# Kernel tuning notes

Measured on AMD Instinct MI355X. Metric: run time of the kernel, lower is better.

## Reference

```python
import jax, jax.numpy as jnp
import numpy as np

NX, NY = 512, 512
FNUM, GNUM = 120, 120
NA = 1.35
WAVELENGTH = NX * NA / 100.0  # chosen so normalized period = 100
N_LIQUID = 1.44
M_RED = 0.25
LOW_LIGHT_THRES = 1e-3
SRC_STEEP = 8.0
RESIST_STEEP = 30.0
RESIST_INT = 0.225
DOSES = (0.98, 1.0, 1.02)
SRC_GRID = 13

X1 = NX // 2 - FNUM; X2 = NX // 2 + FNUM + 1
Y1 = NY // 2 - GNUM; Y2 = NY // 2 + GNUM + 1
_PER_X = NX / (WAVELENGTH / NA)
_PER_Y = NY / (WAVELENGTH / NA)
NORM_SPEC = _PER_X * _PER_Y
DFMDG = 1.0 / NORM_SPEC
_fm = (np.arange(X1, X2) - NX // 2) / _PER_X
_gm = (np.arange(Y1, Y2) - NY // 2) / _PER_Y
_FM, _GM = np.meshgrid(_fm, _gm)  # 'xy' indexing, shape [2*GNUM+1, 2*FNUM+1]
FM = jnp.asarray(_FM, jnp.float32)
GM = jnp.asarray(_GM, jnp.float32)


def cal_pupil(fg2):
    # obliquity factor; pupil phase is identically zero in this module
    num = 1.0 - (M_RED ** 2) * (NA ** 2) * fg2
    den = 1.0 - (NA / N_LIQUID) ** 2 * fg2
    return jnp.sqrt(jnp.sqrt(num / den))


def setup_inputs() -> dict:
    key = jax.random.key(0)
    g = np.linspace(-1.0, 1.0, SRC_GRID, dtype=np.float32)
    fxg, fyg = np.meshgrid(g, g)
    r = np.sqrt(fxg ** 2 + fyg ** 2)
    data = ((r >= 0.6) & (r <= 0.9)).astype(np.float32)  # annular source
    # sigmoid activation init: +1 where lit, -1 elsewhere (zeros, set 2 where data>0.5, sub 1)
    params = 2.0 * data - 1.0
    mask_value = jax.random.uniform(key, (NY, NX), jnp.float32)
    return {
        "mask_value": mask_value,
        "source_params": jnp.asarray(params, jnp.float32),
        "source_fx": jnp.asarray(fxg.reshape(-1), jnp.float32),
        "source_fy": jnp.asarray(fyg.reshape(-1), jnp.float32),
    }


def _forward(mask_value, source_params, source_fx, source_fy):
    # source activation + low-light pruning (masked_select expressed as zero-weighting)
    val = jax.nn.sigmoid(SRC_STEEP * source_params).reshape(-1)  # [S]
    valid = val >= LOW_LIGHT_THRES
    w = jnp.where(valid, val, 0.0)
    weight = jnp.sum(w)

    # normalization intensity (detached in the original)
    fxy2 = source_fx ** 2 + source_fy ** 2
    obl = cal_pupil(jnp.where(valid, fxy2, 0.0))
    norm_I = jax.lax.stop_gradient(
        N_LIQUID * DFMDG ** 2 * jnp.sum(w * (NORM_SPEC * obl) ** 2) / weight
    )

    # shifted pupil per source point over the mask frequency window
    F = FM[None, :, :] + source_fx[:, None, None]  # [S, Gy, Gx]
    G = GM[None, :, :] + source_fy[:, None, None]
    rho2 = F * F + G * G                            # == mask_fg2m + 2(fx*fm+fy*gm) + fxy2
    vmask = rho2 <= 1.0
    pupil = jnp.where(vmask, cal_pupil(jnp.where(vmask, rho2, 0.0)), 0.0)  # [S, Gy, Gx]

    S = w.shape[0]
    Is, Rs = [], []
    for d in DOSES:
        fv = jnp.fft.fftshift(jnp.fft.fft2(jnp.fft.ifftshift(mask_value * d)))
        win = fv[Y1:Y2, X1:X2]                      # [Gy, Gx] complex
        tempH = win[None, :, :] * pupil.astype(jnp.complex64)  # masked spectrum*pupil
        e = jnp.zeros((S, NY, NX), jnp.complex64).at[:, Y1:Y2, X1:X2].set(tempH)
        AA = jnp.fft.fftshift(jnp.fft.ifft2(e), axes=(-2, -1))
        I2 = AA.real ** 2 + AA.imag ** 2            # |AA * conj(AA)|
        intensity = jnp.einsum('s,syx->yx', w, I2) / weight / norm_I
        Is.append(intensity)
        Rs.append(jax.nn.sigmoid(RESIST_STEEP * (intensity - RESIST_INT)))
    # [2, 3, NY, NX]: [0] = aerial intensity per dose, [1] = resist image per dose
    return jnp.stack([jnp.stack(Is), jnp.stack(Rs)])


def reference(mask_value, source_params, source_fx, source_fy):
    return _forward(mask_value, source_params, source_fx, source_fy)
```

## Files before the change

### kernel.cpp

```cpp
#include <hip/hip_runtime.h>
#include <hip/hip_fp16.h>


#define SPLIT 8

static const size_t O_BAR  = 4096;
static const size_t O_ACC  = 32768;
static const size_t ACC_BYTES = (size_t)SPLIT * 512 * 512 * 4;
static const size_t O_WIN  = O_ACC + ACC_BYTES;
static const size_t O_R1   = O_WIN + 464896;
static const size_t O_T2   = O_R1 + 987136;
static const size_t SLOT_BYTES = (size_t)512 * 244 * 4;

__device__ inline void st_sys_f(float* p, float v) {
  __hip_atomic_store((unsigned*)p, __float_as_uint(v),
                     __ATOMIC_RELAXED, __HIP_MEMORY_SCOPE_SYSTEM);
}
__device__ inline float ld_sys_f(const float* p) {
  return __uint_as_float(__hip_atomic_load((const unsigned*)p,
                     __ATOMIC_RELAXED, __HIP_MEMORY_SCOPE_SYSTEM));
}
__device__ inline void st_sys_i(int* p, int v) {
  __hip_atomic_store(p, v, __ATOMIC_RELAXED, __HIP_MEMORY_SCOPE_SYSTEM);
}
__device__ inline int ld_sys_i(const int* p) {
  return __hip_atomic_load(p, __ATOMIC_RELAXED, __HIP_MEMORY_SCOPE_SYSTEM);
}
__device__ inline void st_sys_f2(float2* p, float2 v) {
  union { float2 f; unsigned long long u; } c; c.f = v;
  __hip_atomic_store((unsigned long long*)p, c.u,
                     __ATOMIC_RELAXED, __HIP_MEMORY_SCOPE_SYSTEM);
}
__device__ inline float2 ld_sys_f2(const float2* p) {
  union { unsigned long long u; float2 f; } c;
  c.u = __hip_atomic_load((const unsigned long long*)p,
                     __ATOMIC_RELAXED, __HIP_MEMORY_SCOPE_SYSTEM);
  return c.f;
}
__device__ inline void st_sys_f4(void* p, float4 v) {
  union { float2 f; unsigned long long u; } a, b;
  a.f = make_float2(v.x, v.y); b.f = make_float2(v.z, v.w);
  unsigned long long* q = (unsigned long long*)p;
  __hip_atomic_store(q,     a.u, __ATOMIC_RELAXED, __HIP_MEMORY_SCOPE_SYSTEM);
  __hip_atomic_store(q + 1, b.u, __ATOMIC_RELAXED, __HIP_MEMORY_SCOPE_SYSTEM);
}
__device__ inline __half2 ld_sys_h2(const __half2* p) {
  union { unsigned u; __half2 h; } c;
  c.u = __hip_atomic_load((const unsigned*)p,
                     __ATOMIC_RELAXED, __HIP_MEMORY_SCOPE_SYSTEM);
  return c.h;
}

__device__ inline float2 cadd(float2 a, float2 b){ return make_float2(a.x+b.x, a.y+b.y); }
__device__ inline float2 csub(float2 a, float2 b){ return make_float2(a.x-b.x, a.y-b.y); }
__device__ inline float2 cmul(float2 a, float2 b){
  return make_float2(fmaf(a.x, b.x, -(a.y*b.y)), fmaf(a.x, b.y, a.y*b.x));
}
__device__ inline float2 twsgn(float2 t, int S) {
  return make_float2(t.x, (S > 0) ? t.y : -t.y);
}

__device__ inline void gbar(char* bar, unsigned nblk, unsigned& ep) {
  __syncthreads();
  ep++;
  if (threadIdx.x == 0) {
    const unsigned target = ep;
    const unsigned g    = blockIdx.x >> 5;
    const unsigned ngrp = nblk >> 5;
    unsigned* gcnt = (unsigned*)(bar + (size_t)g * 256);
    unsigned* ggen = (unsigned*)(bar + 8192 + (size_t)g * 256);
    unsigned* rcnt = (unsigned*)(bar + 16384);
    unsigned* rgen = (unsigned*)(bar + 16640);
    asm volatile("s_waitcnt vmcnt(0)" ::: "memory");
    unsigned old = __hip_atomic_fetch_add(gcnt, 1u, __ATOMIC_RELAXED,
                                          __HIP_MEMORY_SCOPE_SYSTEM);
    if (old == 31u) {
      __hip_atomic_store(gcnt, 0u, __ATOMIC_RELAXED, __HIP_MEMORY_SCOPE_SYSTEM);
      unsigned r = __hip_atomic_fetch_add(rcnt, 1u, __ATOMIC_RELAXED,
                                          __HIP_MEMORY_SCOPE_SYSTEM);
      if (r == ngrp - 1u) {
        __hip_atomic_store(rcnt, 0u, __ATOMIC_RELAXED, __HIP_MEMORY_SCOPE_SYSTEM);
        __hip_atomic_store(rgen, target, __ATOMIC_RELAXED,
                           __HIP_MEMORY_SCOPE_SYSTEM);
      } else {
        while (__hip_atomic_load(rgen, __ATOMIC_RELAXED,
                                 __HIP_MEMORY_SCOPE_SYSTEM) < target)
          __builtin_amdgcn_s_sleep(1);
      }
      __hip_atomic_store(ggen, target, __ATOMIC_RELAXED,
                         __HIP_MEMORY_SCOPE_SYSTEM);
    } else {
      while (__hip_atomic_load(ggen, __ATOMIC_RELAXED,
                               __HIP_MEMORY_SCOPE_SYSTEM) < target)
        __builtin_amdgcn_s_sleep(2);
    }
  }
  __syncthreads();
}

__device__ inline void build_twt(float2* twt) {
  for (int k = (int)threadIdx.x; k < 512; k += 256) {
    double a = 6.283185307179586476925286766559 * (double)k / 512.0;
    twt[k] = make_float2((float)cos(a), (float)sin(a));
  }
}

template<int S, bool ZTOP>
__device__ inline void dft8(float2 v[8]) {
  const float sg = (float)S;
  const float C7 = 0.7071067811865476f;
  float2 t0, t1, t2, t3, t4, t5, t6, t7;
  if (ZTOP) {
    t0 = v[0]; t4 = v[0];
    t1 = v[1]; t5 = v[1];
    t2 = v[2]; t6 = v[2];
    t3 = v[3]; t7 = v[3];
  } else {
    t0=cadd(v[0],v[4]); t4=csub(v[0],v[4]);
    t1=cadd(v[1],v[5]); t5=csub(v[1],v[5]);
    t2=cadd(v[2],v[6]); t6=csub(v[2],v[6]);
    t3=cadd(v[3],v[7]); t7=csub(v[3],v[7]);
  }
  t5 = make_float2(C7*(t5.x - sg*t5.y), C7*(t5.y + sg*t5.x));
  t6 = make_float2(-sg*t6.y, sg*t6.x);
  t7 = make_float2(C7*(-t7.x - sg*t7.y), C7*(sg*t7.x - t7.y));
  float2 u0=cadd(t0,t2), u2=csub(t0,t2);
  float2 u1=cadd(t1,t3), u3=csub(t1,t3);
  u3 = make_float2(-sg*u3.y, sg*u3.x);
  float2 u4=cadd(t4,t6), u6=csub(t4,t6);
  float2 u5=cadd(t5,t7), u7=csub(t5,t7);
  u7 = make_float2(-sg*u7.y, sg*u7.x);
  v[0]=cadd(u0,u1); v[4]=csub(u0,u1);
  v[2]=cadd(u2,u3); v[6]=csub(u2,u3);
  v[1]=cadd(u4,u5); v[5]=csub(u4,u5);
  v[3]=cadd(u6,u7); v[7]=csub(u6,u7);
}

template<int S, bool ZTOP>
__device__ inline void wfft512(float2 v[8], int lane, float2* xch,
                               const float2* twt) {
  const int p2 = lane & 7, u0 = lane >> 3;
  dft8<S, ZTOP>(v);
  { float2 t1 = twsgn(twt[lane], S), acc = t1;
    v[1] = cmul(v[1], acc);
    #pragma unroll
    for (int u = 2; u < 8; u++) { acc = cmul(acc, t1); v[u] = cmul(v[u], acc); } }
  __builtin_amdgcn_wave_barrier();
  #pragma unroll
  for (int u = 0; u < 8; u++) xch[u*68 + p2*8 + u0] = v[u];
  __builtin_amdgcn_wave_barrier();
  { const float4* rp = (const float4*)(xch + u0*68 + p2*8);
    #pragma unroll
    for (int q = 0; q < 4; q++) {
      float4 t = rp[q];
      v[2*q]   = make_float2(t.x, t.y);
      v[2*q+1] = make_float2(t.z, t.w);
    } }
  dft8<S, false>(v);
  { float2 t1 = twsgn(twt[p2 << 3], S), acc = t1;
    v[1] = cmul(v[1], acc);
    #pragma unroll
    for (int u = 2; u < 8; u++) { acc = cmul(acc, t1); v[u] = cmul(v[u], acc); } }
  __builtin_amdgcn_wave_barrier();
  #pragma unroll
  for (int u = 0; u < 8; u++) xch[u*68 + lane] = v[u];
  __builtin_amdgcn_wave_barrier();
  { const float4* rp = (const float4*)(xch + p2*68 + u0*8);
    #pragma unroll
    for (int q = 0; q < 4; q++) {
      float4 t = rp[q];
      v[2*q]   = make_float2(t.x, t.y);
      v[2*q+1] = make_float2(t.z, t.w);
    } }
  dft8<S, false>(v);
}

__global__ void __launch_bounds__(256, 4)
k_fused(const float* __restrict__ mask, const float* __restrict__ prm,
        const float* __restrict__ sfx, const float* __restrict__ sfy,
        char* ws, float2* R1t, float2* Wg, __half2* T2, float* acc,
        float* out, int CH) {
  const int t = threadIdx.x, lane = t & 63, wv = t >> 6;
  const unsigned nblk = gridDim.x;
  char* bar = ws + O_BAR;
  unsigned ep = 0;
  __shared__ __align__(16) float2 lds[4*544];
  __shared__ __align__(16) float2 twt[512];
  __shared__ float FMt[241];
  build_twt(twt);
  if (t < 241) FMt[t] = (float)(((double)(t - 120)) / 100.0);
  float2* const xch = lds + wv*544;

  if (blockIdx.x == 0) {
    float*  sw  = (float*)lds;
    float*  sxx = sw + 192; float* syy = sxx + 192; float* scw = syy + 192;
    double* so  = (double*)(sw + 768);
    int*    skp = (int*)(so + 176);
    if (t < 169) {
      float p = prm[t];
      float val = 1.f / (1.f + __expf(-8.f * p));
      float w = (val >= 0.001f) ? val : 0.f;
      double o = 0.0; float fx = 0.f, fy = 0.f;
      if (w > 0.f) {
        fx = sfx[t]; fy = sfy[t];
        double f2 = (double)fx*(double)fx + (double)fy*(double)fy;
        o = (double)w * sqrt((1.0 - 0.11390625 * f2) / (1.0 - 0.87890625 * f2));
      }
      sw[t] = w; so[t] = o; sxx[t] = fx; syy[t] = fy;
    }
    __syncthreads();
    if (t < 169) {
      float w = sw[t];
      int keep = 0; float cw = w;
      if (w > 0.f) {
        float fx = sxx[t], fy = syy[t];
        int pr = -1;
        for (int s2 = 0; s2 < 169; s2++) {
          if (sw[s2] > 0.f && fabsf(sxx[s2] + fx) < 1e-5f
                           && fabsf(syy[s2] + fy) < 1e-5f) { pr = s2; break; }
        }
        if (pr < 0 || pr == t) keep = 1;
        else if (pr > t) { keep = 1; cw = w + sw[pr]; }
      }
      skp[t] = keep; scw[t] = cw;
    }
    __syncthreads();
    if (t == 0) {
      float* wsfw = (float*)ws;
      double Sden = 0.0; int c = 0;
      for (int s = 0; s < 169; s++) {
        Sden += so[s];
        if (skp[s]) {
          st_sys_f(wsfw + 64 + c,  scw[s]);
          st_sys_f(wsfw + 320 + c, sxx[s]);
          st_sys_f(wsfw + 576 + c, syy[s]);
          c++;
        }
      }
      st_sys_i((int*)ws, c);
      st_sys_f(wsfw + 1, (float)(1.0 / (262144.0 * 1.44 * Sden)));
    }
    __syncthreads();
  }
  {
    int rb0, step;
    if (nblk > 128) { rb0 = (int)blockIdx.x - 1; step = (int)nblk - 1; }
    else            { rb0 = (int)blockIdx.x;     step = (int)nblk; }
    if (rb0 >= 0) {
      for (int rb = rb0; rb < 128; rb += step) {
        int y = rb * 4 + wv;
        float2 v[8];
        #pragma unroll
        for (int q = 0; q < 8; q++) v[q] = make_float2(mask[y*512 + 64*q + lane], 0.f);
        wfft512<-1, false>(v, lane, xch, twt);
        #pragma unroll
        for (int u = 0; u < 8; u++) {
          int k = (lane>>3) + 8*(lane&7) + 64*u;
          int beta = (k >= 392) ? (k - 392) : ((k <= 120) ? (k + 120) : -1);
          if (beta >= 0) st_sys_f2(R1t + beta*512 + y, v[u]);
        }
      }
    }
  }
  gbar(bar, nblk, ep);

  for (int jb = blockIdx.x; jb < 61; jb += nblk) {
    int j = jb * 4 + wv;
    float2 v[8];
    #pragma unroll
    for (int q = 0; q < 8; q++)
      v[q] = (j < 241) ? ld_sys_f2(R1t + j*512 + 64*q + lane)
                       : make_float2(0.f, 0.f);
    wfft512<-1, false>(v, lane, xch, twt);
    if (j < 241) {
      #pragma unroll
      for (int u = 0; u < 8; u++) {
        int k = (lane>>3) + 8*(lane&7) + 64*u;
        int alpha = (k >= 392) ? (k - 392) : ((k <= 120) ? (k + 120) : -1);
        if (alpha >= 0) st_sys_f2(Wg + alpha*241 + j, v[u]);
      }
    }
  }
  gbar(bar, nblk, ep);

  const float* wsf = (const float*)ws;
  const int count = ld_sys_i((const int*)ws);
  int nb = (count + CH - 1) / CH;
  if (nb < 1) nb = 1;
  for (int bi = 0; bi < nb; bi++) {
    const int base = bi * CH;
    int active = count - base;
    if (active > CH) active = CH;
    if (active < 0) active = 0;
    const int ntask = active * 31;

    for (int task = blockIdx.x; task < ntask; task += nblk) {
      int sic  = task / 31;
      int tile = task % 31;
      int slot = base + sic;
      float fx = ld_sys_f(wsf + 320 + slot), fy = ld_sys_f(wsf + 576 + slot);
      float sqw = __fsqrt_rn(ld_sys_f(wsf + 64 + slot)) * 0.001953125f;
      #pragma unroll
      for (int ph = 0; ph < 2; ph++) {
        int alpha = tile*8 + ph*4 + wv;
        bool arow = (alpha < 241);
        float Gf = __fadd_rn(arow ? FMt[alpha] : 0.f, fy);
        float g2 = __fmul_rn(Gf, Gf);
        bool active_row = arow && (g2 <= 1.0f);
        float2 v[8];
        #pragma unroll
        for (int q = 0; q < 8; q++) v[q] = make_float2(0.f, 0.f);
        if (active_row) {
          #pragma unroll
          for (int q = 0; q < 4; q++) {
            int n = 64*q + lane;
            if (n < 241) {
              float Ff = __fadd_rn(FMt[n], fx);
              float r2 = __fadd_rn(__fmul_rn(Ff, Ff), g2);
              if (r2 <= 1.0f) {
                float num = fmaf(-0.11390625f, r2, 1.0f);
                float den = fmaf(-0.87890625f, r2, 1.0f);
                float P = __fsqrt_rn(__fsqrt_rn(__fdividef(num, den))) * sqw;
                float2 Wv = ld_sys_f2(Wg + alpha*241 + n);
                v[q] = make_float2(P * Wv.x, P * Wv.y);
              }
            }
          }
          wfft512<1, true>(v, lane, xch, twt);
        }
        #pragma unroll
        for (int u = 0; u < 8; u++) {
          int xx = (lane>>3) + 8*(lane&7) + 64*u;
          xch[xx] = v[u];
        }
        __syncthreads();
        int colb = tile*8 + ph*4;
        if (colb < 244) {
          #pragma unroll
          for (int r = 0; r < 2; r++) {
            int x = t + 256*r;
            union { __half2 h[4]; float4 f; } uu;
            #pragma unroll
            for (int wvi = 0; wvi < 4; wvi++) {
              float2 a = lds[wvi*544 + x];
              uu.h[wvi] = __floats2half2_rn(a.x, a.y);
            }
            st_sys_f4(T2 + ((size_t)sic*512 + x)*244 + colb, uu.f);
          }
        }
        __syncthreads();
      }
    }
    gbar(bar, nblk, ep);

    for (int unit = blockIdx.x; unit < 1024; unit += nblk) {
      int part = unit & 7;
      int x = (unit >> 3) * 4 + wv;
      float av[8] = {0.f,0.f,0.f,0.f,0.f,0.f,0.f,0.f};
      int sic = part;
      bool act = (sic < CH) && (base + sic < count);
      __half2 pv[4] = {{0.f,0.f},{0.f,0.f},{0.f,0.f},{0.f,0.f}};
      if (act) {
        const __half2* row = T2 + ((size_t)sic*512 + x)*244;
        #pragma unroll
        for (int q = 0; q < 4; q++) {
          int n = 64*q + lane;
          pv[q] = (n < 241) ? ld_sys_h2(row + n) : __half2{0.f, 0.f};
        }
      }
      while (act) {
        float2 v[8];
        #pragma unroll
        for (int q = 0; q < 4; q++) v[q] = __half22float2(pv[q]);
        #pragma unroll
        for (int q = 4; q < 8; q++) v[q] = make_float2(0.f, 0.f);
        int nsic = sic + SPLIT;
        act = (nsic < CH) && (base + nsic < count);
        if (act) {
          const __half2* row = T2 + ((size_t)nsic*512 + x)*244;
          #pragma unroll
          for (int q = 0; q < 4; q++) {
            int n = 64*q + lane;
            pv[q] = (n < 241) ? ld_sys_h2(row + n) : __half2{0.f, 0.f};
          }
        }
        wfft512<1, true>(v, lane, xch, twt);
        #pragma unroll
        for (int u = 0; u < 8; u++)
          av[u] += fmaf(v[u].x, v[u].x, v[u].y*v[u].y);
        sic = nsic;
      }
      float* a = acc + ((size_t)part << 18) + (size_t)x * 512;
      int y0 = (lane>>3) + 8*(lane&7);
      if (bi == 0) {
        #pragma unroll
        for (int u = 0; u < 8; u++) st_sys_f(a + y0 + 64*u, av[u]);
      } else {
        #pragma unroll
        for (int u = 0; u < 8; u++) {
          float prev = ld_sys_f(a + y0 + 64*u);
          st_sys_f(a + y0 + 64*u, prev + av[u]);
        }
      }
    }
    gbar(bar, nblk, ep);
  }

  {
    float scale = ld_sys_f(wsf + 1);
    float (*tile2)[33] = reinterpret_cast<float(*)[33]>((float*)lds);
    const float dd[3] = {0.9604f, 1.0f, 1.0404f};
    int tx = t & 31, ty0 = t >> 5;
    for (int tb = blockIdx.x; tb < 256; tb += nblk) {
      int x0 = (tb & 15) * 32, y0 = (tb >> 4) * 32;
      #pragma unroll
      for (int r = 0; r < 4; r++) {
        int i = ty0 + 8*r;
        const float* ap = acc + (size_t)(x0 + i)*512 + y0 + tx;
        float s = 0.f;
        #pragma unroll
        for (int p = 0; p < SPLIT; p++) s += ld_sys_f(ap + ((size_t)p << 18));
        tile2[i][tx] = s;
      }
      __syncthreads();
      #pragma unroll
      for (int r = 0; r < 4; r++) {
        int yy = ty0 + 8*r;
        float I = scale * tile2[tx][yy];
        int o = (y0 + yy)*512 + x0 + tx;
        #pragma unroll
        for (int d = 0; d < 3; d++) {
          float Ik = dd[d] * I;
          out[(size_t)d*262144 + o] = Ik;
          out[(size_t)(3+d)*262144 + o] = 1.f / (1.f + __expf(-30.f*(Ik - 0.225f)));
        }
      }
      __syncthreads();
    }
  }
}

extern "C" void kernel_launch(void* const* d_in, const int* in_sizes, int n_in,
                              void* d_out, int out_size, void* d_ws, size_t ws_size,
                              hipStream_t stream) {
  (void)in_sizes; (void)n_in; (void)out_size;
  const float* mask = (const float*)d_in[0];
  const float* prm  = (const float*)d_in[1];
  const float* sfx  = (const float*)d_in[2];
  const float* sfy  = (const float*)d_in[3];
  float* out = (float*)d_out;
  char*  ws  = (char*)d_ws;

  float*   acc = (float*)(ws + O_ACC);
  float2*  Wg  = (float2*)(ws + O_WIN);
  float2*  R1t = (float2*)(ws + O_R1);
  __half2* T2  = (__half2*)(ws + O_T2);

  size_t avail = (ws_size > O_T2) ? (ws_size - O_T2) : 0;
  int CH = (int)(avail / SLOT_BYTES);
  if (CH > 169) CH = 169;
  if (CH < 1)   CH = 1;

  static int grid_blocks = 0;
  if (grid_blocks == 0) {
    int nbk = 0;
    if (hipOccupancyMaxActiveBlocksPerMultiprocessor(
            &nbk, (const void*)k_fused, 256, 0) != hipSuccess || nbk < 1)
      nbk = 1;
    if (nbk > 1) nbk -= 1;
    int ncu = 256;
    hipDeviceProp_t prop;
    int dev = 0;
    if (hipGetDevice(&dev) == hipSuccess &&
        hipGetDeviceProperties(&prop, dev) == hipSuccess &&
        prop.multiProcessorCount > 0)
      ncu = prop.multiProcessorCount;
    long g = (long)nbk * (long)ncu;
    if (g > 1024) g = 1024;
    g &= ~31L;
    if (g < 32) g = 32;
    grid_blocks = (int)g;
  }

  hipMemsetAsync(ws + O_BAR, 0, 24576, stream);

  k_fused<<<dim3(grid_blocks), dim3(256), 0, stream>>>(
      mask, prm, sfx, sfy, ws, R1t, Wg, T2, acc, out, CH);
}
```

Measured before the change: 152.1 us.

## Coalesce global stores via LDS transposes and widen T2 row layout

Routes the R1t and Wg transpose writes through LDS so each thread stores contiguous runs instead of strided scattered 8-byte stores. The stage-3 task split is reorganised so each block processes one column group of 4 per wave over 64 tasks, and the T2 row pitch is padded to 256 so stage-4 loads become 16-byte contiguous per lane. Accumulator writes and the final reduction are also vectorised to float2 after an LDS reshuffle. This adds extra LDS traffic and barriers, and changes task granularity, which may affect load balance.

Result: slower. 159.7 us (+5.0%).

```diff
diff --git a/kernel.cpp b/kernel.cpp
--- a/kernel.cpp
+++ b/kernel.cpp
@@ -10,7 +10,7 @@
 static const size_t O_WIN  = O_ACC + ACC_BYTES;
 static const size_t O_R1   = O_WIN + 464896;
 static const size_t O_T2   = O_R1 + 987136;
-static const size_t SLOT_BYTES = (size_t)512 * 244 * 4;
+static const size_t SLOT_BYTES = (size_t)512 * 256 * 4;
 
 __device__ inline void st_sys_f(float* p, float v) {
   __hip_atomic_store((unsigned*)p, __float_as_uint(v),
@@ -36,6 +36,10 @@
   c.u = __hip_atomic_load((const unsigned long long*)p,
                      __ATOMIC_RELAXED, __HIP_MEMORY_SCOPE_SYSTEM);
   return c.f;
+}
+__device__ inline unsigned long long ld_sys_u64(const void* p) {
+  return __hip_atomic_load((const unsigned long long*)p,
+                     __ATOMIC_RELAXED, __HIP_MEMORY_SCOPE_SYSTEM);
 }
 __device__ inline void st_sys_f4(void* p, float4 v) {
   union { float2 f; unsigned long long u; } a, b;
@@ -43,12 +47,6 @@
   unsigned long long* q = (unsigned long long*)p;
   __hip_atomic_store(q,     a.u, __ATOMIC_RELAXED, __HIP_MEMORY_SCOPE_SYSTEM);
   __hip_atomic_store(q + 1, b.u, __ATOMIC_RELAXED, __HIP_MEMORY_SCOPE_SYSTEM);
-}
-__device__ inline __half2 ld_sys_h2(const __half2* p) {
-  union { unsigned u; __half2 h; } c;
-  c.u = __hip_atomic_load((const unsigned*)p,
-                     __ATOMIC_RELAXED, __HIP_MEMORY_SCOPE_SYSTEM);
-  return c.h;
 }
 
 __device__ inline float2 cadd(float2 a, float2 b){ return make_float2(a.x+b.x, a.y+b.y); }
@@ -191,6 +189,7 @@
   if (t < 241) FMt[t] = (float)(((double)(t - 120)) / 100.0);
   float2* const xch = lds + wv*544;
 
+  __syncthreads();
   if (blockIdx.x == 0) {
     float*  sw  = (float*)lds;
     float*  sxx = sw + 192; float* syy = sxx + 192; float* scw = syy + 192;
@@ -257,8 +256,15 @@
         for (int u = 0; u < 8; u++) {
           int k = (lane>>3) + 8*(lane&7) + 64*u;
           int beta = (k >= 392) ? (k - 392) : ((k <= 120) ? (k + 120) : -1);
-          if (beta >= 0) st_sys_f2(R1t + beta*512 + y, v[u]);
-        }
+          if (beta >= 0) xch[beta] = v[u];
+        }
+        __syncthreads();
+        if (t < 241) {
+          float2* dst = R1t + t*512 + rb*4;
+          #pragma unroll
+          for (int w = 0; w < 4; w++) st_sys_f2(dst + w, lds[w*544 + t]);
+        }
+        __syncthreads();
       }
     }
   }
@@ -272,14 +278,21 @@
       v[q] = (j < 241) ? ld_sys_f2(R1t + j*512 + 64*q + lane)
                        : make_float2(0.f, 0.f);
     wfft512<-1, false>(v, lane, xch, twt);
-    if (j < 241) {
-      #pragma unroll
-      for (int u = 0; u < 8; u++) {
-        int k = (lane>>3) + 8*(lane&7) + 64*u;
-        int alpha = (k >= 392) ? (k - 392) : ((k <= 120) ? (k + 120) : -1);
-        if (alpha >= 0) st_sys_f2(Wg + alpha*241 + j, v[u]);
-      }
-    }
+    #pragma unroll
+    for (int u = 0; u < 8; u++) {
+      int k = (lane>>3) + 8*(lane&7) + 64*u;
+      int alpha = (k >= 392) ? (k - 392) : ((k <= 120) ? (k + 120) : -1);
+      if (alpha >= 0) xch[alpha] = v[u];
+    }
+    __syncthreads();
+    {
+      int nj = 241 - jb*4; if (nj > 4) nj = 4;
+      if (t < 241) {
+        float2* dst = Wg + t*241 + jb*4;
+        for (int w = 0; w < nj; w++) st_sys_f2(dst + w, lds[w*544 + t]);
+      }
+    }
+    __syncthreads();
   }
   gbar(bar, nblk, ep);
 
@@ -292,97 +305,85 @@
     int active = count - base;
     if (active > CH) active = CH;
     if (active < 0) active = 0;
-    const int ntask = active * 31;
+    const int ntask = active * 64;
 
     for (int task = blockIdx.x; task < ntask; task += nblk) {
-      int sic  = task / 31;
-      int tile = task % 31;
+      int sic = task >> 6;
+      int g   = task & 63;
       int slot = base + sic;
       float fx = ld_sys_f(wsf + 320 + slot), fy = ld_sys_f(wsf + 576 + slot);
       float sqw = __fsqrt_rn(ld_sys_f(wsf + 64 + slot)) * 0.001953125f;
+      int alpha = 64*wv + g;
+      bool arow = (alpha < 241);
+      float Gf = __fadd_rn(arow ? FMt[alpha] : 0.f, fy);
+      float g2 = __fmul_rn(Gf, Gf);
+      bool active_row = arow && (g2 <= 1.0f);
+      float2 v[8];
       #pragma unroll
-      for (int ph = 0; ph < 2; ph++) {
-        int alpha = tile*8 + ph*4 + wv;
-        bool arow = (alpha < 241);
-        float Gf = __fadd_rn(arow ? FMt[alpha] : 0.f, fy);
-        float g2 = __fmul_rn(Gf, Gf);
-        bool active_row = arow && (g2 <= 1.0f);
-        float2 v[8];
-        #pragma unroll
-        for (int q = 0; q < 8; q++) v[q] = make_float2(0.f, 0.f);
-        if (active_row) {
-          #pragma unroll
-          for (int q = 0; q < 4; q++) {
-            int n = 64*q + lane;
-            if (n < 241) {
-              float Ff = __fadd_rn(FMt[n], fx);
-              float r2 = __fadd_rn(__fmul_rn(Ff, Ff), g2);
-              if (r2 <= 1.0f) {
-                float num = fmaf(-0.11390625f, r2, 1.0f);
-                float den = fmaf(-0.87890625f, r2, 1.0f);
-                float P = __fsqrt_rn(__fsqrt_rn(__fdividef(num, den))) * sqw;
-                float2 Wv = ld_sys_f2(Wg + alpha*241 + n);
-                v[q] = make_float2(P * Wv.x, P * Wv.y);
-              }
+      for (int q = 0; q < 8; q++) v[q] = make_float2(0.f, 0.f);
+      if (active_row) {
+        #pragma unroll
+        for (int q = 0; q < 4; q++) {
+          int n = 64*q + lane;
+          if (n < 241) {
+            float Ff = __fadd_rn(FMt[n], fx);
+            float r2 = __fadd_rn(__fmul_rn(Ff, Ff), g2);
+            if (r2 <= 1.0f) {
+              float num = fmaf(-0.11390625f, r2, 1.0f);
+              float den = fmaf(-0.87890625f, r2, 1.0f);
+              float P = __fsqrt_rn(__fsqrt_rn(__fdividef(num, den))) * sqw;
+              float2 Wv = ld_sys_f2(Wg + alpha*241 + n);
+              v[q] = make_float2(P * Wv.x, P * Wv.y);
             }
           }
-          wfft512<1, true>(v, lane, xch, twt);
-        }
-        #pragma unroll
-        for (int u = 0; u < 8; u++) {
-          int xx = (lane>>3) + 8*(lane&7) + 64*u;
-          xch[xx] = v[u];
-        }
-        __syncthreads();
-        int colb = tile*8 + ph*4;
-        if (colb < 244) {
-          #pragma unroll
-          for (int r = 0; r < 2; r++) {
-            int x = t + 256*r;
-            union { __half2 h[4]; float4 f; } uu;
-            #pragma unroll
-            for (int wvi = 0; wvi < 4; wvi++) {
-              float2 a = lds[wvi*544 + x];
-              uu.h[wvi] = __floats2half2_rn(a.x, a.y);
-            }
-            st_sys_f4(T2 + ((size_t)sic*512 + x)*244 + colb, uu.f);
-          }
-        }
-        __syncthreads();
-      }
+        }
+        wfft512<1, true>(v, lane, xch, twt);
+      }
+      #pragma unroll
+      for (int u = 0; u < 8; u++) {
+        int xx = (lane>>3) + 8*(lane&7) + 64*u;
+        xch[xx] = v[u];
+      }
+      __syncthreads();
+      #pragma unroll
+      for (int r = 0; r < 2; r++) {
+        int x = t + 256*r;
+        union { __half2 h[4]; float4 f; } uu;
+        #pragma unroll
+        for (int wvi = 0; wvi < 4; wvi++) {
+          float2 a = lds[wvi*544 + x];
+          uu.h[wvi] = __floats2half2_rn(a.x, a.y);
+        }
+        st_sys_f4(T2 + ((size_t)sic*512 + x)*256 + 4*g, uu.f);
+      }
+      __syncthreads();
     }
     gbar(bar, nblk, ep);
 
-    for (int unit = blockIdx.x; unit < 1024; unit += nblk) {
-      int part = unit & 7;
+    for (int unit = blockIdx.x; unit < 128*SPLIT; unit += nblk) {
+      int part = unit & (SPLIT-1);
       int x = (unit >> 3) * 4 + wv;
       float av[8] = {0.f,0.f,0.f,0.f,0.f,0.f,0.f,0.f};
       int sic = part;
       bool act = (sic < CH) && (base + sic < count);
-      __half2 pv[4] = {{0.f,0.f},{0.f,0.f},{0.f,0.f},{0.f,0.f}};
+      unsigned long long pvlo = 0ull, pvhi = 0ull;
       if (act) {
-        const __half2* row = T2 + ((size_t)sic*512 + x)*244;
-        #pragma unroll
-        for (int q = 0; q < 4; q++) {
-          int n = 64*q + lane;
-          pv[q] = (n < 241) ? ld_sys_h2(row + n) : __half2{0.f, 0.f};
-        }
+        const char* rb8 = (const char*)T2 + ((size_t)sic*512 + x)*1024 + 16*lane;
+        pvlo = ld_sys_u64(rb8); pvhi = ld_sys_u64(rb8 + 8);
       }
       while (act) {
+        union { unsigned long long u[2]; __half2 h[4]; } cur;
+        cur.u[0] = pvlo; cur.u[1] = pvhi;
         float2 v[8];
         #pragma unroll
-        for (int q = 0; q < 4; q++) v[q] = __half22float2(pv[q]);
+        for (int q = 0; q < 4; q++) v[q] = __half22float2(cur.h[q]);
         #pragma unroll
         for (int q = 4; q < 8; q++) v[q] = make_float2(0.f, 0.f);
         int nsic = sic + SPLIT;
         act = (nsic < CH) && (base + nsic < count);
         if (act) {
-          const __half2* row = T2 + ((size_t)nsic*512 + x)*244;
-          #pragma unroll
-          for (int q = 0; q < 4; q++) {
-            int n = 64*q + lane;
-            pv[q] = (n < 241) ? ld_sys_h2(row + n) : __half2{0.f, 0.f};
-          }
+          const char* rb8 = (const char*)T2 + ((size_t)nsic*512 + x)*1024 + 16*lane;
+          pvlo = ld_sys_u64(rb8); pvhi = ld_sys_u64(rb8 + 8);
         }
         wfft512<1, true>(v, lane, xch, twt);
         #pragma unroll
@@ -390,17 +391,26 @@
           av[u] += fmaf(v[u].x, v[u].x, v[u].y*v[u].y);
         sic = nsic;
       }
-      float* a = acc + ((size_t)part << 18) + (size_t)x * 512;
-      int y0 = (lane>>3) + 8*(lane&7);
-      if (bi == 0) {
-        #pragma unroll
-        for (int u = 0; u < 8; u++) st_sys_f(a + y0 + 64*u, av[u]);
-      } else {
-        #pragma unroll
-        for (int u = 0; u < 8; u++) {
-          float prev = ld_sys_f(a + y0 + 64*u);
-          st_sys_f(a + y0 + 64*u, prev + av[u]);
-        }
+      {
+        float* xf = (float*)xch;
+        int y0 = (lane>>3) + 8*(lane&7);
+        #pragma unroll
+        for (int u = 0; u < 8; u++) xf[y0 + 64*u] = av[u];
+        __builtin_amdgcn_wave_barrier();
+        float* a = acc + ((size_t)part << 18) + (size_t)x * 512 + 8*lane;
+        if (bi == 0) {
+          #pragma unroll
+          for (int k = 0; k < 4; k++)
+            st_sys_f2((float2*)a + k, *(float2*)(xf + 8*lane + 2*k));
+        } else {
+          #pragma unroll
+          for (int k = 0; k < 4; k++) {
+            float2 pr = ld_sys_f2((float2*)a + k);
+            float2 vl = *(float2*)(xf + 8*lane + 2*k);
+            st_sys_f2((float2*)a + k, make_float2(pr.x + vl.x, pr.y + vl.y));
+          }
+        }
+        __builtin_amdgcn_wave_barrier();
       }
     }
     gbar(bar, nblk, ep);
@@ -411,16 +421,20 @@
     float (*tile2)[33] = reinterpret_cast<float(*)[33]>((float*)lds);
     const float dd[3] = {0.9604f, 1.0f, 1.0404f};
     int tx = t & 31, ty0 = t >> 5;
+    int yq = (t & 15) * 2, i0d = t >> 4;
     for (int tb = blockIdx.x; tb < 256; tb += nblk) {
       int x0 = (tb & 15) * 32, y0 = (tb >> 4) * 32;
       #pragma unroll
-      for (int r = 0; r < 4; r++) {
-        int i = ty0 + 8*r;
-        const float* ap = acc + (size_t)(x0 + i)*512 + y0 + tx;
-        float s = 0.f;
-        #pragma unroll
-        for (int p = 0; p < SPLIT; p++) s += ld_sys_f(ap + ((size_t)p << 18));
-        tile2[i][tx] = s;
+      for (int r = 0; r < 2; r++) {
+        int i = i0d + 16*r;
+        const float* ap = acc + (size_t)(x0 + i)*512 + y0 + yq;
+        float sx = 0.f, sy = 0.f;
+        #pragma unroll
+        for (int p = 0; p < SPLIT; p++) {
+          float2 vv = ld_sys_f2((const float2*)(ap + ((size_t)p << 18)));
+          sx += vv.x; sy += vv.y;
+        }
+        tile2[i][yq] = sx; tile2[i][yq+1] = sy;
       }
       __syncthreads();
       #pragma unroll
```

## Use plain cached loads/stores for T2 and acc with cache-flushing grid barrier

Applied to the files above, without the earlier changes.

Replaces system-scope atomic loads and stores on the T2 intermediate and accumulator buffers with ordinary cached accesses. A new barrier adds a per-XCC writeback fence between the two global barriers, intended to keep data coherent across XCCs. It also pads T2 rows to 256 columns so the tiling covers 16 column blocks of 16 with aligned float4 stores. The risk is coherence bugs if the fence scheme misses any path, and the extra barrier adds latency.

Result: slower. 157.9 us (+3.8%).

```diff
diff --git a/kernel.cpp b/kernel.cpp
--- a/kernel.cpp
+++ b/kernel.cpp
@@ -10,7 +10,7 @@
 static const size_t O_WIN  = O_ACC + ACC_BYTES;
 static const size_t O_R1   = O_WIN + 464896;
 static const size_t O_T2   = O_R1 + 987136;
-static const size_t SLOT_BYTES = (size_t)512 * 244 * 4;
+static const size_t SLOT_BYTES = (size_t)512 * 256 * 4;
 
 __device__ inline void st_sys_f(float* p, float v) {
   __hip_atomic_store((unsigned*)p, __float_as_uint(v),
@@ -36,19 +36,6 @@
   c.u = __hip_atomic_load((const unsigned long long*)p,
                      __ATOMIC_RELAXED, __HIP_MEMORY_SCOPE_SYSTEM);
   return c.f;
-}
-__device__ inline void st_sys_f4(void* p, float4 v) {
-  union { float2 f; unsigned long long u; } a, b;
-  a.f = make_float2(v.x, v.y); b.f = make_float2(v.z, v.w);
-  unsigned long long* q = (unsigned long long*)p;
-  __hip_atomic_store(q,     a.u, __ATOMIC_RELAXED, __HIP_MEMORY_SCOPE_SYSTEM);
-  __hip_atomic_store(q + 1, b.u, __ATOMIC_RELAXED, __HIP_MEMORY_SCOPE_SYSTEM);
-}
-__device__ inline __half2 ld_sys_h2(const __half2* p) {
-  union { unsigned u; __half2 h; } c;
-  c.u = __hip_atomic_load((const unsigned*)p,
-                     __ATOMIC_RELAXED, __HIP_MEMORY_SCOPE_SYSTEM);
-  return c.h;
 }
 
 __device__ inline float2 cadd(float2 a, float2 b){ return make_float2(a.x+b.x, a.y+b.y); }
@@ -96,6 +83,18 @@
     }
   }
   __syncthreads();
+}
+
+__device__ inline void fbar(char* bar, unsigned nblk, unsigned& ep) {
+  gbar(bar, nblk, ep);
+  if (threadIdx.x == 0) {
+    unsigned xcc = __builtin_amdgcn_s_getreg(63508) & 7u;
+    unsigned* cw = (unsigned*)(bar + 17408) + (size_t)ep * 8 + xcc;
+    if (__hip_atomic_exchange(cw, 1u, __ATOMIC_RELAXED,
+                              __HIP_MEMORY_SCOPE_SYSTEM) == 0u)
+      __threadfence();
+  }
+  gbar(bar, nblk, ep);
 }
 
 __device__ inline void build_twt(float2* twt) {
@@ -191,6 +190,7 @@
   if (t < 241) FMt[t] = (float)(((double)(t - 120)) / 100.0);
   float2* const xch = lds + wv*544;
 
+  __syncthreads();
   if (blockIdx.x == 0) {
     float*  sw  = (float*)lds;
     float*  sxx = sw + 192; float* syy = sxx + 192; float* scw = syy + 192;
@@ -292,17 +292,18 @@
     int active = count - base;
     if (active > CH) active = CH;
     if (active < 0) active = 0;
-    const int ntask = active * 31;
+    const int ntask = active * 16;
 
     for (int task = blockIdx.x; task < ntask; task += nblk) {
-      int sic  = task / 31;
-      int tile = task % 31;
+      int sic = task >> 4;
+      int lb  = task & 15;
       int slot = base + sic;
       float fx = ld_sys_f(wsf + 320 + slot), fy = ld_sys_f(wsf + 576 + slot);
       float sqw = __fsqrt_rn(ld_sys_f(wsf + 64 + slot)) * 0.001953125f;
       #pragma unroll
-      for (int ph = 0; ph < 2; ph++) {
-        int alpha = tile*8 + ph*4 + wv;
+      for (int r = 0; r < 4; r++) {
+        int colb  = lb*16 + r*4;
+        int alpha = colb + wv;
         bool arow = (alpha < 241);
         float Gf = __fadd_rn(arow ? FMt[alpha] : 0.f, fy);
         float g2 = __fmul_rn(Gf, Gf);
@@ -334,38 +335,35 @@
           xch[xx] = v[u];
         }
         __syncthreads();
-        int colb = tile*8 + ph*4;
-        if (colb < 244) {
+        #pragma unroll
+        for (int rr = 0; rr < 2; rr++) {
+          int x = t + 256*rr;
+          union { __half2 h[4]; float4 f; } uu;
           #pragma unroll
-          for (int r = 0; r < 2; r++) {
-            int x = t + 256*r;
-            union { __half2 h[4]; float4 f; } uu;
-            #pragma unroll
-            for (int wvi = 0; wvi < 4; wvi++) {
-              float2 a = lds[wvi*544 + x];
-              uu.h[wvi] = __floats2half2_rn(a.x, a.y);
-            }
-            st_sys_f4(T2 + ((size_t)sic*512 + x)*244 + colb, uu.f);
+          for (int wvi = 0; wvi < 4; wvi++) {
+            float2 a = lds[wvi*544 + x];
+            uu.h[wvi] = __floats2half2_rn(a.x, a.y);
           }
+          *(float4*)(T2 + ((size_t)sic*512 + x)*256 + colb) = uu.f;
         }
         __syncthreads();
       }
     }
-    gbar(bar, nblk, ep);
-
-    for (int unit = blockIdx.x; unit < 1024; unit += nblk) {
-      int part = unit & 7;
+    fbar(bar, nblk, ep);
+
+    for (int unit = blockIdx.x; unit < 128*SPLIT; unit += nblk) {
+      int part = unit & (SPLIT-1);
       int x = (unit >> 3) * 4 + wv;
       float av[8] = {0.f,0.f,0.f,0.f,0.f,0.f,0.f,0.f};
       int sic = part;
       bool act = (sic < CH) && (base + sic < count);
       __half2 pv[4] = {{0.f,0.f},{0.f,0.f},{0.f,0.f},{0.f,0.f}};
       if (act) {
-        const __half2* row = T2 + ((size_t)sic*512 + x)*244;
+        const __half2* row = T2 + ((size_t)sic*512 + x)*256;
         #pragma unroll
         for (int q = 0; q < 4; q++) {
           int n = 64*q + lane;
-          pv[q] = (n < 241) ? ld_sys_h2(row + n) : __half2{0.f, 0.f};
+          pv[q] = (n < 241) ? row[n] : __half2{0.f, 0.f};
         }
       }
       while (act) {
@@ -377,11 +375,11 @@
         int nsic = sic + SPLIT;
         act = (nsic < CH) && (base + nsic < count);
         if (act) {
-          const __half2* row = T2 + ((size_t)nsic*512 + x)*244;
+          const __half2* row = T2 + ((size_t)nsic*512 + x)*256;
           #pragma unroll
           for (int q = 0; q < 4; q++) {
             int n = 64*q + lane;
-            pv[q] = (n < 241) ? ld_sys_h2(row + n) : __half2{0.f, 0.f};
+            pv[q] = (n < 241) ? row[n] : __half2{0.f, 0.f};
           }
         }
         wfft512<1, true>(v, lane, xch, twt);
@@ -394,16 +392,13 @@
       int y0 = (lane>>3) + 8*(lane&7);
       if (bi == 0) {
         #pragma unroll
-        for (int u = 0; u < 8; u++) st_sys_f(a + y0 + 64*u, av[u]);
+        for (int u = 0; u < 8; u++) a[y0 + 64*u] = av[u];
       } else {
         #pragma unroll
-        for (int u = 0; u < 8; u++) {
-          float prev = ld_sys_f(a + y0 + 64*u);
-          st_sys_f(a + y0 + 64*u, prev + av[u]);
-        }
-      }
-    }
-    gbar(bar, nblk, ep);
+        for (int u = 0; u < 8; u++) a[y0 + 64*u] += av[u];
+      }
+    }
+    fbar(bar, nblk, ep);
   }
 
   {
@@ -419,7 +414,7 @@
         const float* ap = acc + (size_t)(x0 + i)*512 + y0 + tx;
         float s = 0.f;
         #pragma unroll
-        for (int p = 0; p < SPLIT; p++) s += ld_sys_f(ap + ((size_t)p << 18));
+        for (int p = 0; p < SPLIT; p++) s += ap[(size_t)p << 18];
         tile2[i][tx] = s;
       }
       __syncthreads();
@@ -482,7 +477,7 @@
     grid_blocks = (int)g;
   }
 
-  hipMemsetAsync(ws + O_BAR, 0, 24576, stream);
+  hipMemsetAsync(ws + O_BAR, 0, 28672, stream);
 
   k_fused<<<dim3(grid_blocks), dim3(256), 0, stream>>>(
       mask, prm, sfx, sfy, ws, R1t, Wg, T2, acc, out, CH);
```
